# Optimization experiments

Measured on AMD Instinct MI355X. Metric: run time of the kernel, lower is better.

## Reference

```python
import jax, jax.numpy as jnp
import numpy as np

B, T, I, H, O = 65536, 50, 2, 20, 2
P_DROP = 0.2


def setup_inputs() -> dict:
    key = jax.random.key(0)
    ks = jax.random.split(key, 8)
    s = 1.0 / np.sqrt(H)  # torch nn.RNN / nn.Linear uniform init bound
    u = lambda k, shape: jax.random.uniform(k, shape, jnp.float32, -s, s)
    x = jax.random.normal(ks[0], (B, T, I), jnp.float32)
    W_ih = u(ks[1], (H, I))
    W_hh = u(ks[2], (H, H))
    b_ih = u(ks[3], (H,))
    b_hh = u(ks[4], (H,))
    W_out = u(ks[5], (O, H))
    b_out = u(ks[6], (O,))
    # MC-dropout mask (training-mode dropout, inverted scaling), fixed for determinism
    keep = jax.random.uniform(ks[7], (B, T, H)) >= P_DROP
    drop_mask = keep.astype(jnp.float32) / (1.0 - P_DROP)
    return {"x": x, "W_ih": W_ih, "W_hh": W_hh, "b_ih": b_ih, "b_hh": b_hh,
            "W_out": W_out, "b_out": b_out, "drop_mask": drop_mask}


def reference(x, W_ih, W_hh, b_ih, b_hh, W_out, b_out, drop_mask):
    # Precompute input projection for all timesteps in one big GEMM: [B,T,H]
    xp = jnp.einsum('bti,hi->bth', x, W_ih) + b_ih + b_hh

    def step(h, xt):  # h: [B,H], xt: [B,H]
        h_new = jnp.tanh(xt + h @ W_hh.T)
        return h_new, h_new

    h0 = jnp.zeros((x.shape[0], W_hh.shape[0]), x.dtype)
    _, hs = jax.lax.scan(step, h0, jnp.swapaxes(xp, 0, 1))  # hs: [T,B,H]
    r_out = jnp.swapaxes(hs, 0, 1)  # [B,T,H]
    out = (r_out * drop_mask) @ W_out.T + b_out  # [B,T,O]
    return out
```

## Files before the change

### kernel.cpp

```cpp
#include <hip/hip_runtime.h>

#ifndef __has_builtin
#define __has_builtin(x) 0
#endif

#if __has_builtin(__builtin_amdgcn_exp2f)
#define EXP2F(x) __builtin_amdgcn_exp2f(x)
#else
#define EXP2F(x) exp2f(x)
#endif

#if __has_builtin(__builtin_amdgcn_rcpf)
#define RCPF(x) __builtin_amdgcn_rcpf(x)
#else
#define RCPF(x) (1.0f / (x))
#endif

namespace {

constexpr int kB = 65536;
constexpr int kT = 50;
constexpr int kI = 2;
constexpr int kH = 20;
constexpr int kO = 2;
constexpr int kGB = 64;

__device__ __forceinline__ float fast_tanh(float v) {
    const float p = EXP2F(v * 2.8853900817779268f);
    return fmaf(-2.0f, RCPF(p + 1.0f), 1.0f);
}

#if __has_builtin(__builtin_amdgcn_mov_dpp)
template <int CTRL>
__device__ __forceinline__ float fqp(float v) {
    return __int_as_float(
        __builtin_amdgcn_mov_dpp(__float_as_int(v), CTRL, 0xF, 0xF, true));
}
#else
template <int CTRL>
__device__ __forceinline__ float fqp(float v) {
    constexpr int d = (CTRL == 0xB1) ? 1 : (CTRL == 0x4E) ? 2 : 3;
    return __shfl_xor(v, d);
}
#endif

__global__ __launch_bounds__(256)
__attribute__((amdgpu_waves_per_eu(2, 4)))
void dprnn_kernel(
    const float* __restrict__ x, const float* __restrict__ W_ih,
    const float* __restrict__ W_hh, const float* __restrict__ b_ih,
    const float* __restrict__ b_hh, const float* __restrict__ W_out,
    const float* __restrict__ b_out, const float* __restrict__ mask,
    float* __restrict__ out)
{
    __shared__ __align__(16) float lds_o[kGB * kT * kO];

    const int tidx = threadIdx.x;
    const int gl   = tidx >> 2;
    const int sub  = tidx & 3;
    const size_t g = (size_t)blockIdx.x * kGB + gl;

    float w[5][5][4];
    float wi0[5], wi1[5], bia[5], wo0[5], wo1[5];
#pragma unroll
    for (int i = 0; i < 5; ++i) {
        const int row = 4 * i + sub;
#pragma unroll
        for (int r = 0; r < 5; ++r)
#pragma unroll
            for (int d = 0; d < 4; ++d)
                w[i][r][d] = W_hh[row * kH + 4 * r + (sub ^ d)];
        wi0[i] = W_ih[row * kI + 0];
        wi1[i] = W_ih[row * kI + 1];
        bia[i] = b_ih[row] + b_hh[row];
        wo0[i] = W_out[row];
        wo1[i] = W_out[kH + row];
    }
    const float bo0 = b_out[0];
    const float bo1 = b_out[1];

    float h[5] = {0.f, 0.f, 0.f, 0.f, 0.f};

    const float* mp = mask + g * (kT * kH) + sub;
    const float* xp = x + g * (kT * kI);

    auto step = [&](const float* m, float x0, float x1, int t) {
        float acc[5];
#pragma unroll
        for (int i = 0; i < 5; ++i)
            acc[i] = fmaf(wi0[i], x0, fmaf(wi1[i], x1, bia[i]));
#pragma unroll
        for (int r = 0; r < 5; ++r) {
            const float v0 = h[r];
            const float v1 = fqp<0xB1>(h[r]);
            const float v2 = fqp<0x4E>(h[r]);
            const float v3 = fqp<0x1B>(h[r]);
#pragma unroll
            for (int i = 0; i < 5; ++i) {
                acc[i] = fmaf(w[i][r][0], v0, acc[i]);
                acc[i] = fmaf(w[i][r][1], v1, acc[i]);
                acc[i] = fmaf(w[i][r][2], v2, acc[i]);
                acc[i] = fmaf(w[i][r][3], v3, acc[i]);
            }
        }
        float p0 = 0.f, p1 = 0.f;
#pragma unroll
        for (int i = 0; i < 5; ++i) {
            const float hn = fast_tanh(acc[i]);
            h[i] = hn;
            const float dm = hn * m[i];
            p0 = fmaf(dm, wo0[i], p0);
            p1 = fmaf(dm, wo1[i], p1);
        }
        p0 += fqp<0xB1>(p0);
        p0 += fqp<0x4E>(p0);
        p1 += fqp<0xB1>(p1);
        p1 += fqp<0x4E>(p1);
        if (sub == 0)
            *(float2*)&lds_o[gl * (kT * kO) + t * kO] =
                make_float2(p0 + bo0, p1 + bo1);
    };

    float mP[10], mQ[10];
    float4 xP, xQ;

    auto load_pair_P = [&](int p) {
        const float* q = mp + p * (2 * kH);
#pragma unroll
        for (int r = 0; r < 5; ++r) {
            mP[r]     = q[4 * r];
            mP[5 + r] = q[kH + 4 * r];
        }
        xP = *(const float4*)(xp + p * 4);
    };
    auto load_pair_Q = [&](int p) {
        const float* q = mp + p * (2 * kH);
#pragma unroll
        for (int r = 0; r < 5; ++r) {
            mQ[r]     = q[4 * r];
            mQ[5 + r] = q[kH + 4 * r];
        }
        xQ = *(const float4*)(xp + p * 4);
    };

    load_pair_P(0);
    load_pair_Q(1);

#pragma unroll 1
    for (int it = 0; it < 12; ++it) {
        const int e = 2 * it;
        step(&mP[0], xP.x, xP.y, e * 2);
        step(&mP[5], xP.z, xP.w, e * 2 + 1);
        load_pair_P(e + 2);

        const int o = e + 1;
        step(&mQ[0], xQ.x, xQ.y, o * 2);
        step(&mQ[5], xQ.z, xQ.w, o * 2 + 1);
        if (it < 11) load_pair_Q(o + 2);
    }
    step(&mP[0], xP.x, xP.y, 48);
    step(&mP[5], xP.z, xP.w, 49);

    __syncthreads();
    float* ob = out + (size_t)blockIdx.x * (kGB * kT * kO);
#pragma unroll
    for (int it = 0; it < 6; ++it) {
        const int idx = it * 1024 + tidx * 4;
        const float4 v = *(const float4*)&lds_o[idx];
        *(float4*)(ob + idx) = v;
    }
    {
        const int idx = 6144 + tidx;
        ob[idx] = lds_o[idx];
    }
}

}

extern "C" void kernel_launch(void* const* d_in, const int* in_sizes, int n_in,
                              void* d_out, int out_size, void* d_ws, size_t ws_size,
                              hipStream_t stream) {
    const float* x     = (const float*)d_in[0];
    const float* W_ih  = (const float*)d_in[1];
    const float* W_hh  = (const float*)d_in[2];
    const float* b_ih  = (const float*)d_in[3];
    const float* b_hh  = (const float*)d_in[4];
    const float* W_out = (const float*)d_in[5];
    const float* b_out = (const float*)d_in[6];
    const float* mask  = (const float*)d_in[7];
    float* out = (float*)d_out;

    dim3 block(256);
    dim3 grid(kB / kGB);
    dprnn_kernel<<<grid, block, 0, stream>>>(x, W_ih, W_hh, b_ih, b_hh,
                                             W_out, b_out, mask, out);
}
```

Measured before the change: 93.27 us.

## Stage dropout mask through LDS with coalesced float4 loads, write outputs directly

Each wave now loads its 16 batch rows of the dropout mask in contiguous float4 chunks of four timesteps. The chunks are written into a double-buffered LDS area, replacing per-thread strided scalar global loads. Each step reads its mask values from LDS, with a separate tail load for the last two timesteps. Output staging through LDS and the final block copy are removed, so results are stored as scattered float2 writes straight to global memory. The occupancy hint is also pinned to 2 waves per EU. The aim is better mask-read coalescing and more bytes in flight, at the cost of less coalesced output stores and extra LDS traffic.

```diff
diff --git a/kernel.cpp b/kernel.cpp
--- a/kernel.cpp
+++ b/kernel.cpp
@@ -24,6 +24,9 @@
 constexpr int kH = 20;
 constexpr int kO = 2;
 constexpr int kGB = 64;
+constexpr int kES  = 84;
+constexpr int kBUF = kGB * kES;
+constexpr int kBUF_B = kBUF * 4;
 
 __device__ __forceinline__ float fast_tanh(float v) {
     const float p = EXP2F(v * 2.8853900817779268f);
@@ -44,8 +47,26 @@
 }
 #endif
 
+#define LOADSET(S, c)                                                  \
+    {                                                                  \
+        S##0 = *(const float4*)(mblk + so0 + (c) * 320);               \
+        S##1 = *(const float4*)(mblk + so1 + (c) * 320);               \
+        S##2 = *(const float4*)(mblk + so2 + (c) * 320);               \
+        S##3 = *(const float4*)(mblk + so3 + (c) * 320);               \
+        S##4 = *(const float4*)(mblk + so4 + (c) * 320);               \
+    }
+
+#define WRITESET(S, bufbyte)                                           \
+    {                                                                  \
+        *(float4*)(smb + (bufbyte) + lo0) = S##0;                      \
+        *(float4*)(smb + (bufbyte) + lo1) = S##1;                      \
+        *(float4*)(smb + (bufbyte) + lo2) = S##2;                      \
+        *(float4*)(smb + (bufbyte) + lo3) = S##3;                      \
+        *(float4*)(smb + (bufbyte) + lo4) = S##4;                      \
+    }
+
 __global__ __launch_bounds__(256)
-__attribute__((amdgpu_waves_per_eu(2, 4)))
+__attribute__((amdgpu_waves_per_eu(2, 2)))
 void dprnn_kernel(
     const float* __restrict__ x, const float* __restrict__ W_ih,
     const float* __restrict__ W_hh, const float* __restrict__ b_ih,
@@ -53,11 +74,14 @@
     const float* __restrict__ b_out, const float* __restrict__ mask,
     float* __restrict__ out)
 {
-    __shared__ __align__(16) float lds_o[kGB * kT * kO];
+    __shared__ __align__(16) float sm[2 * kBUF];
+    char* smb = (char*)sm;
 
     const int tidx = threadIdx.x;
     const int gl   = tidx >> 2;
     const int sub  = tidx & 3;
+    const int Wv   = tidx >> 6;
+    const int l    = tidx & 63;
     const size_t g = (size_t)blockIdx.x * kGB + gl;
 
     float w[5][5][4];
@@ -79,12 +103,44 @@
     const float bo0 = b_out[0];
     const float bo1 = b_out[1];
 
+    const char* mblk = (const char*)mask + (size_t)blockIdx.x * kGB * 4000;
+    uint32_t so0, so1, so2, so3, so4, lo0, lo1, lo2, lo3, lo4;
+    {
+        int p, e, o;
+        p = 0 * 64 + l; e = p / 20; o = p - 20 * e;
+        so0 = (Wv * 16 + e) * 4000 + o * 16; lo0 = (Wv * 16 + e) * 336 + o * 16;
+        p = 1 * 64 + l; e = p / 20; o = p - 20 * e;
+        so1 = (Wv * 16 + e) * 4000 + o * 16; lo1 = (Wv * 16 + e) * 336 + o * 16;
+        p = 2 * 64 + l; e = p / 20; o = p - 20 * e;
+        so2 = (Wv * 16 + e) * 4000 + o * 16; lo2 = (Wv * 16 + e) * 336 + o * 16;
+        p = 3 * 64 + l; e = p / 20; o = p - 20 * e;
+        so3 = (Wv * 16 + e) * 4000 + o * 16; lo3 = (Wv * 16 + e) * 336 + o * 16;
+        p = 4 * 64 + l; e = p / 20; o = p - 20 * e;
+        so4 = (Wv * 16 + e) * 4000 + o * 16; lo4 = (Wv * 16 + e) * 336 + o * 16;
+    }
+    uint32_t tso0, tso1, tso2, tlo0, tlo1, tlo2;
+    {
+        int p, e, o;
+        p = 0 * 64 + l;                   e = p / 10; o = p - 10 * e;
+        tso0 = (Wv * 16 + e) * 4000 + 3840 + o * 16; tlo0 = (Wv * 16 + e) * 336 + o * 16;
+        p = 1 * 64 + l;                   e = p / 10; o = p - 10 * e;
+        tso1 = (Wv * 16 + e) * 4000 + 3840 + o * 16; tlo1 = (Wv * 16 + e) * 336 + o * 16;
+        p = 2 * 64 + l; p = (p > 159) ? 159 : p; e = p / 10; o = p - 10 * e;
+        tso2 = (Wv * 16 + e) * 4000 + 3840 + o * 16; tlo2 = (Wv * 16 + e) * 336 + o * 16;
+    }
+
+    const float* xp = x + g * (kT * kI);
+    float* op = out + g * (kT * kO);
+    const int mrd = gl * kES + sub;
+
     float h[5] = {0.f, 0.f, 0.f, 0.f, 0.f};
 
-    const float* mp = mask + g * (kT * kH) + sub;
-    const float* xp = x + g * (kT * kI);
-
-    auto step = [&](const float* m, float x0, float x1, int t) {
+    auto step = [&](int off, float x0, float x1, int t) {
+        const float m0_ = sm[mrd + off];
+        const float m1_ = sm[mrd + off + 4];
+        const float m2_ = sm[mrd + off + 8];
+        const float m3_ = sm[mrd + off + 12];
+        const float m4_ = sm[mrd + off + 16];
         float acc[5];
 #pragma unroll
         for (int i = 0; i < 5; ++i)
@@ -103,12 +159,13 @@
                 acc[i] = fmaf(w[i][r][3], v3, acc[i]);
             }
         }
+        const float mm[5] = {m0_, m1_, m2_, m3_, m4_};
         float p0 = 0.f, p1 = 0.f;
 #pragma unroll
         for (int i = 0; i < 5; ++i) {
             const float hn = fast_tanh(acc[i]);
             h[i] = hn;
-            const float dm = hn * m[i];
+            const float dm = hn * mm[i];
             p0 = fmaf(dm, wo0[i], p0);
             p1 = fmaf(dm, wo1[i], p1);
         }
@@ -117,62 +174,63 @@
         p1 += fqp<0xB1>(p1);
         p1 += fqp<0x4E>(p1);
         if (sub == 0)
-            *(float2*)&lds_o[gl * (kT * kO) + t * kO] =
-                make_float2(p0 + bo0, p1 + bo1);
+            *(float2*)(op + t * kO) = make_float2(p0 + bo0, p1 + bo1);
     };
 
-    float mP[10], mQ[10];
-    float4 xP, xQ;
-
-    auto load_pair_P = [&](int p) {
-        const float* q = mp + p * (2 * kH);
-#pragma unroll
-        for (int r = 0; r < 5; ++r) {
-            mP[r]     = q[4 * r];
-            mP[5 + r] = q[kH + 4 * r];
+    float4 A0, A1, A2, A3, A4;
+    float4 B0, B1, B2, B3, B4;
+    float4 Ta, Tb, Tc, xT;
+
+    LOADSET(A, 0);
+    LOADSET(B, 1);
+    float4 xE0 = *(const float4*)(xp);
+    float4 xE1 = *(const float4*)(xp + 4);
+    float4 xO0 = *(const float4*)(xp + 8);
+    float4 xO1 = *(const float4*)(xp + 12);
+    WRITESET(A, 0);
+    LOADSET(A, 2);
+
+#pragma unroll 1
+    for (int k = 0; k < 12; ++k) {
+        if ((k & 1) == 0) {
+            WRITESET(B, kBUF_B);
+            if (k <= 8) LOADSET(B, (k + 3));
+            step(0,  xE0.x, xE0.y, 4 * k);
+            step(20, xE0.z, xE0.w, 4 * k + 1);
+            step(40, xE1.x, xE1.y, 4 * k + 2);
+            step(60, xE1.z, xE1.w, 4 * k + 3);
+            if (k <= 8) {
+                xE0 = *(const float4*)(xp + 8 * (k + 2));
+                xE1 = *(const float4*)(xp + 8 * (k + 2) + 4);
+            }
+        } else {
+            if (k == 11) {
+                *(float4*)(smb + tlo0) = Ta;
+                *(float4*)(smb + tlo1) = Tb;
+                *(float4*)(smb + tlo2) = Tc;
+            } else {
+                WRITESET(A, 0);
+            }
+            if (k <= 8) LOADSET(A, (k + 3));
+            if (k == 9) {
+                Ta = *(const float4*)(mblk + tso0);
+                Tb = *(const float4*)(mblk + tso1);
+                Tc = *(const float4*)(mblk + tso2);
+                xT = *(const float4*)(xp + 96);
+            }
+            step(kBUF,      xO0.x, xO0.y, 4 * k);
+            step(kBUF + 20, xO0.z, xO0.w, 4 * k + 1);
+            step(kBUF + 40, xO1.x, xO1.y, 4 * k + 2);
+            step(kBUF + 60, xO1.z, xO1.w, 4 * k + 3);
+            if (k <= 9) {
+                xO0 = *(const float4*)(xp + 8 * (k + 2));
+                xO1 = *(const float4*)(xp + 8 * (k + 2) + 4);
+            }
         }
-        xP = *(const float4*)(xp + p * 4);
-    };
-    auto load_pair_Q = [&](int p) {
-        const float* q = mp + p * (2 * kH);
-#pragma unroll
-        for (int r = 0; r < 5; ++r) {
-            mQ[r]     = q[4 * r];
-            mQ[5 + r] = q[kH + 4 * r];
-        }
-        xQ = *(const float4*)(xp + p * 4);
-    };
-
-    load_pair_P(0);
-    load_pair_Q(1);
-
-#pragma unroll 1
-    for (int it = 0; it < 12; ++it) {
-        const int e = 2 * it;
-        step(&mP[0], xP.x, xP.y, e * 2);
-        step(&mP[5], xP.z, xP.w, e * 2 + 1);
-        load_pair_P(e + 2);
-
-        const int o = e + 1;
-        step(&mQ[0], xQ.x, xQ.y, o * 2);
-        step(&mQ[5], xQ.z, xQ.w, o * 2 + 1);
-        if (it < 11) load_pair_Q(o + 2);
-    }
-    step(&mP[0], xP.x, xP.y, 48);
-    step(&mP[5], xP.z, xP.w, 49);
-
-    __syncthreads();
-    float* ob = out + (size_t)blockIdx.x * (kGB * kT * kO);
-#pragma unroll
-    for (int it = 0; it < 6; ++it) {
-        const int idx = it * 1024 + tidx * 4;
-        const float4 v = *(const float4*)&lds_o[idx];
-        *(float4*)(ob + idx) = v;
-    }
-    {
-        const int idx = 6144 + tidx;
-        ob[idx] = lds_o[idx];
-    }
+    }
+
+    step(0,  xT.x, xT.y, 48);
+    step(20, xT.z, xT.w, 49);
 }
 
 }
```

After: 180.7 us. +93.7%, slower.
